# Optimization experiments

Hardware: AMD Instinct MI355X
Metric: run time of the kernel (lower is better)

## Reference

```python
import jax, jax.numpy as jnp
import numpy as np

B, C, H, W = 8, 64, 112, 112
O, K, PAD, STRIDE = 64, 3, 1, 1
KK = K * K
OH = (H - K + 2 * PAD) // STRIDE + 1
OW = (W - K + 2 * PAD) // STRIDE + 1
L = OH * OW  # number of patches


def setup_inputs() -> dict:
    key = jax.random.key(0)
    k1, k2, k3 = jax.random.split(key, 3)
    x = jax.random.normal(k1, (B, C, H, W), dtype=jnp.float32)
    weight = jax.random.normal(k2, (O, C, K, K), dtype=jnp.float32)
    # one uniformly random kernel position to zero out, per patch (nums=1)
    mask_idx = jax.random.randint(k3, (L,), 0, KK, dtype=jnp.int32)
    return {"x": x, "weight": weight, "mask_idx": mask_idx}


def reference(x, weight, mask_idx):
    b = x.shape[0]
    # im2col: [b, C*KK, OH, OW], feature dim ordered channel-major (c, kh, kw)
    # which matches torch.nn.Unfold ordering.
    patches = jax.lax.conv_general_dilated_patches(
        x, (K, K), (STRIDE, STRIDE), ((PAD, PAD), (PAD, PAD)))
    patches = patches.reshape(b, C * KK, L)  # [b, CK, L]

    # Per-patch mask over kernel positions, tiled across channels
    # (equivalent to mask.repeat(1, in_channels) in the original).
    mask = jnp.ones((L, KK), dtype=x.dtype).at[jnp.arange(L), mask_idx].set(0.0)
    mask_full = jnp.tile(mask, (1, C))  # [L, C*KK]

    # weight.view(O, -1).t() -> [CK, O]; masking the weight rows per patch is
    # mathematically identical to masking the unfolded input per patch, which
    # avoids materializing the [L, CK, O] masked weight tensor.
    w2 = weight.reshape(O, C * KK).T  # [CK, O]
    out = jnp.einsum('bkl,lk,ko->bol', patches, mask_full, w2)  # [b, O, L]
    return out.reshape(b, O, OH, OW)
```

## Files before the change

kernel.cpp:

```cpp
#include <hip/hip_runtime.h>
#include <hip/hip_bf16.h>
#include <cstdint>

#define Bn 8
#define Cn 64
#define Hn 112
#define Wn 112
#define On 64
#define Ln (Hn * Wn)
#define HP 114
#define WP 114

typedef __attribute__((ext_vector_type(4))) float f32x4;
typedef __attribute__((ext_vector_type(8))) short bf16x8;
typedef __attribute__((ext_vector_type(4))) unsigned int u32x4;

__device__ __forceinline__ unsigned short f2bf(float f) {
    unsigned u = __float_as_uint(f);
    unsigned r = 0x7fffu + ((u >> 16) & 1u);
    return (unsigned short)((u + r) >> 16);
}

__global__ __launch_bounds__(128) void prepad_nhwc(const float* __restrict__ x,
                                                   unsigned short* __restrict__ xpad) {
    int bh = blockIdx.x;
    int b = bh / HP, hp = bh - b * HP;
    int wp = threadIdx.x;
    if (wp >= WP) return;
    int h = hp - 1, w = wp - 1;
    bool inb = (h >= 0) & (h < Hn) & (w >= 0) & (w < Wn);
    const float* src = x + ((size_t)b * Cn) * (Hn * Wn) + (inb ? (h * Wn + w) : 0);
    unsigned int buf[32];
#pragma unroll
    for (int c = 0; c < Cn; c += 2) {
        float v0 = src[(size_t)c * (Hn * Wn)];
        float v1 = src[(size_t)(c + 1) * (Hn * Wn)];
        if (!inb) { v0 = 0.f; v1 = 0.f; }
        buf[c >> 1] = (unsigned)f2bf(v0) | ((unsigned)f2bf(v1) << 16);
    }
    u32x4* dst = reinterpret_cast<u32x4*>(xpad + ((size_t)(b * HP + hp) * WP + wp) * Cn);
#pragma unroll
    for (int i = 0; i < 8; i++) {
        u32x4 v;
        v[0] = buf[i * 4 + 0]; v[1] = buf[i * 4 + 1];
        v[2] = buf[i * 4 + 2]; v[3] = buf[i * 4 + 3];
        dst[i] = v;
    }
}

__global__ __launch_bounds__(64) void wpack_kernel(const float* __restrict__ w,
                                                   unsigned short* __restrict__ wpk) {
    int idx = blockIdx.x;
    int ki = idx & 1, of = (idx >> 1) & 3, p = idx >> 3;
    int lane = threadIdx.x;
    int o = of * 16 + (lane & 15);
    int cb = ki * 32 + (lane >> 4) * 8;
    unsigned int pk[4];
#pragma unroll
    for (int j = 0; j < 4; j++) {
        float v0 = w[((size_t)o * Cn + cb + 2 * j) * 9 + p];
        float v1 = w[((size_t)o * Cn + cb + 2 * j + 1) * 9 + p];
        pk[j] = (unsigned)f2bf(v0) | ((unsigned)f2bf(v1) << 16);
    }
    u32x4 v; v[0] = pk[0]; v[1] = pk[1]; v[2] = pk[2]; v[3] = pk[3];
    reinterpret_cast<u32x4*>(wpk)[idx * 64 + lane] = v;
}

__global__ __launch_bounds__(512) void conv_main(const unsigned short* __restrict__ xpad,
                                                 const unsigned short* __restrict__ wpk,
                                                 const int* __restrict__ mask_idx,
                                                 float* __restrict__ out) {
    __shared__ char xs[4 * WP * Cn * 2];

    int blk = blockIdx.x;
    int b = blk / 98;
    int lt = blk - b * 98;
    int l0 = lt * 128;
    int oh0 = l0 / Wn;

    int tid = threadIdx.x;

    const u32x4* src = reinterpret_cast<const u32x4*>(
        xpad + ((size_t)(b * HP + oh0) * WP) * Cn);
#pragma unroll
    for (int it = 0; it < 8; it++) {
        int idx = tid + it * 512;
        if (idx < 4 * WP * 8) {
            u32x4 v = src[idx];
            int rw = idx >> 3;
            int wq = rw % WP;
            int off = (idx * 16) ^ ((wq & 7) << 4);
            *reinterpret_cast<u32x4*>(xs + off) = v;
        }
    }

    int wave = tid >> 6, lane = tid & 63;
    int wr = wave >> 2;
    int wc = wave & 3;
    int g = lane >> 4, li = lane & 15;

    int pit0 = wc * 32 + li;
    int pit1 = pit0 + 16;
    int lg0 = l0 + pit0, lg1 = l0 + pit1;
    int oh_0 = lg0 / Wn, ow_0 = lg0 - oh_0 * Wn;
    int oh_1 = lg1 / Wn, ow_1 = lg1 - oh_1 * Wn;
    int r0 = oh_0 - oh0, r1 = oh_1 - oh0;
    int mv0 = mask_idx[lg0], mv1 = mask_idx[lg1];

    f32x4 acc[2][2] = {};
    const u32x4* wv = reinterpret_cast<const u32x4*>(wpk);
    const u32x4 vzero = {0u, 0u, 0u, 0u};

    __syncthreads();

    for (int p = 0; p < 9; p++) {
        int dh = p / 3, dw = p - dh * 3;

        bf16x8 af[2][2];
#pragma unroll
        for (int mi = 0; mi < 2; mi++)
#pragma unroll
            for (int ki = 0; ki < 2; ki++) {
                int fidx = p * 8 + (wr * 2 + mi) * 2 + ki;
                u32x4 raw = wv[fidx * 64 + lane];
                af[mi][ki] = *reinterpret_cast<bf16x8*>(&raw);
            }

        int wq0 = ow_0 + dw, wq1 = ow_1 + dw;
        int ba0 = ((((r0 + dh) * WP + wq0) << 7) + (g << 4)) ^ ((wq0 & 7) << 4);
        int ba1 = ((((r1 + dh) * WP + wq1) << 7) + (g << 4)) ^ ((wq1 & 7) << 4);
        u32x4 v00 = *reinterpret_cast<const u32x4*>(xs + ba0);
        u32x4 v01 = *reinterpret_cast<const u32x4*>(xs + (ba0 ^ 64));
        u32x4 v10 = *reinterpret_cast<const u32x4*>(xs + ba1);
        u32x4 v11 = *reinterpret_cast<const u32x4*>(xs + (ba1 ^ 64));
        if (mv0 == p) { v00 = vzero; v01 = vzero; }
        if (mv1 == p) { v10 = vzero; v11 = vzero; }
        bf16x8 bf00 = *reinterpret_cast<bf16x8*>(&v00);
        bf16x8 bf01 = *reinterpret_cast<bf16x8*>(&v01);
        bf16x8 bf10 = *reinterpret_cast<bf16x8*>(&v10);
        bf16x8 bf11 = *reinterpret_cast<bf16x8*>(&v11);

#pragma unroll
        for (int mi = 0; mi < 2; mi++) {
            acc[mi][0] = __builtin_amdgcn_mfma_f32_16x16x32_bf16(af[mi][0], bf00, acc[mi][0], 0, 0, 0);
            acc[mi][0] = __builtin_amdgcn_mfma_f32_16x16x32_bf16(af[mi][1], bf01, acc[mi][0], 0, 0, 0);
            acc[mi][1] = __builtin_amdgcn_mfma_f32_16x16x32_bf16(af[mi][0], bf10, acc[mi][1], 0, 0, 0);
            acc[mi][1] = __builtin_amdgcn_mfma_f32_16x16x32_bf16(af[mi][1], bf11, acc[mi][1], 0, 0, 0);
        }
    }

#pragma unroll
    for (int mi = 0; mi < 2; mi++) {
#pragma unroll
        for (int ni = 0; ni < 2; ni++) {
            int o = wr * 32 + mi * 16 + g * 4;
            int lpix = l0 + wc * 32 + ni * 16 + li;
            float* dst = out + ((size_t)(b * On + o)) * Ln + lpix;
#pragma unroll
            for (int r = 0; r < 4; r++) dst[(size_t)r * Ln] = acc[mi][ni][r];
        }
    }
}

extern "C" void kernel_launch(void* const* d_in, const int* in_sizes, int n_in,
                              void* d_out, int out_size, void* d_ws, size_t ws_size,
                              hipStream_t stream) {
    const float* x    = (const float*)d_in[0];
    const float* w    = (const float*)d_in[1];
    const int*   mask = (const int*)d_in[2];
    float* out = (float*)d_out;

    unsigned short* xpad = (unsigned short*)d_ws;
    unsigned short* wpk  = (unsigned short*)((char*)d_ws +
                                             (size_t)Bn * HP * WP * Cn * 2);

    prepad_nhwc <<<Bn * HP, 128, 0, stream>>>(x, xpad);
    wpack_kernel<<<72,      64,  0, stream>>>(w, wpk);
    conv_main   <<<Bn * 98, 512, 0, stream>>>(xpad, wpk, mask, out);
}
```

Before: 112.8 us.

## Fuse NCHW-to-padded-NHWC bf16 conversion into conv kernel, prefetch weights

Drops the separate prepad kernel. The conv kernel now reads fp32 NCHW input directly, converts it to bf16 and writes the padded, swizzled tile straight into shared memory. This removes a launch and the write-then-read of the padded intermediate buffer, but each input row is loaded redundantly by neighbouring tiles (four rows per 128-pixel tile), and the global reads are strided across channels. The change also software-prefetches the next kernel position's weight fragments into registers, and reorders block indexing so the batch index varies fastest.

```diff
diff --git a/kernel.cpp b/kernel.cpp
--- a/kernel.cpp
+++ b/kernel.cpp
@@ -15,37 +15,10 @@
 typedef __attribute__((ext_vector_type(8))) short bf16x8;
 typedef __attribute__((ext_vector_type(4))) unsigned int u32x4;
 
-__device__ __forceinline__ unsigned short f2bf(float f) {
+__device__ __forceinline__ unsigned f2bf(float f) {
     unsigned u = __float_as_uint(f);
     unsigned r = 0x7fffu + ((u >> 16) & 1u);
-    return (unsigned short)((u + r) >> 16);
-}
-
-__global__ __launch_bounds__(128) void prepad_nhwc(const float* __restrict__ x,
-                                                   unsigned short* __restrict__ xpad) {
-    int bh = blockIdx.x;
-    int b = bh / HP, hp = bh - b * HP;
-    int wp = threadIdx.x;
-    if (wp >= WP) return;
-    int h = hp - 1, w = wp - 1;
-    bool inb = (h >= 0) & (h < Hn) & (w >= 0) & (w < Wn);
-    const float* src = x + ((size_t)b * Cn) * (Hn * Wn) + (inb ? (h * Wn + w) : 0);
-    unsigned int buf[32];
-#pragma unroll
-    for (int c = 0; c < Cn; c += 2) {
-        float v0 = src[(size_t)c * (Hn * Wn)];
-        float v1 = src[(size_t)(c + 1) * (Hn * Wn)];
-        if (!inb) { v0 = 0.f; v1 = 0.f; }
-        buf[c >> 1] = (unsigned)f2bf(v0) | ((unsigned)f2bf(v1) << 16);
-    }
-    u32x4* dst = reinterpret_cast<u32x4*>(xpad + ((size_t)(b * HP + hp) * WP + wp) * Cn);
-#pragma unroll
-    for (int i = 0; i < 8; i++) {
-        u32x4 v;
-        v[0] = buf[i * 4 + 0]; v[1] = buf[i * 4 + 1];
-        v[2] = buf[i * 4 + 2]; v[3] = buf[i * 4 + 3];
-        dst[i] = v;
-    }
+    return (u + r) >> 16;
 }
 
 __global__ __launch_bounds__(64) void wpack_kernel(const float* __restrict__ w,
@@ -60,36 +33,49 @@
     for (int j = 0; j < 4; j++) {
         float v0 = w[((size_t)o * Cn + cb + 2 * j) * 9 + p];
         float v1 = w[((size_t)o * Cn + cb + 2 * j + 1) * 9 + p];
-        pk[j] = (unsigned)f2bf(v0) | ((unsigned)f2bf(v1) << 16);
+        pk[j] = f2bf(v0) | (f2bf(v1) << 16);
     }
     u32x4 v; v[0] = pk[0]; v[1] = pk[1]; v[2] = pk[2]; v[3] = pk[3];
     reinterpret_cast<u32x4*>(wpk)[idx * 64 + lane] = v;
 }
 
-__global__ __launch_bounds__(512) void conv_main(const unsigned short* __restrict__ xpad,
-                                                 const unsigned short* __restrict__ wpk,
-                                                 const int* __restrict__ mask_idx,
-                                                 float* __restrict__ out) {
+__global__ __launch_bounds__(512) void conv_fused(const float* __restrict__ x,
+                                                  const unsigned short* __restrict__ wpk,
+                                                  const int* __restrict__ mask_idx,
+                                                  float* __restrict__ out) {
     __shared__ char xs[4 * WP * Cn * 2];
 
-    int blk = blockIdx.x;
-    int b = blk / 98;
-    int lt = blk - b * 98;
+    int b  = blockIdx.x & 7;
+    int lt = blockIdx.x >> 3;
     int l0 = lt * 128;
     int oh0 = l0 / Wn;
 
     int tid = threadIdx.x;
 
-    const u32x4* src = reinterpret_cast<const u32x4*>(
-        xpad + ((size_t)(b * HP + oh0) * WP) * Cn);
+    const float* xb = x + (size_t)b * Cn * Hn * Wn;
 #pragma unroll
-    for (int it = 0; it < 8; it++) {
-        int idx = tid + it * 512;
-        if (idx < 4 * WP * 8) {
-            u32x4 v = src[idx];
-            int rw = idx >> 3;
-            int wq = rw % WP;
-            int off = (idx * 16) ^ ((wq & 7) << 4);
+    for (int it = 0; it < 8; ++it) {
+        int q = tid + it * 512;
+        if (q < 4 * 8 * WP) {
+            int row = q / (8 * WP);
+            int rem = q - row * (8 * WP);
+            int c8  = rem / WP;
+            int wp  = rem - c8 * WP;
+            int h = oh0 + row - 1;
+            int w = wp - 1;
+            bool inb = ((unsigned)h < (unsigned)Hn) & ((unsigned)w < (unsigned)Wn);
+            const float* s = xb + ((size_t)(c8 * 8) * Hn + (inb ? h : 0)) * Wn + (inb ? w : 0);
+            unsigned pk[4];
+#pragma unroll
+            for (int j = 0; j < 4; ++j) {
+                float v0 = s[(size_t)(2 * j)     * (Hn * Wn)];
+                float v1 = s[(size_t)(2 * j + 1) * (Hn * Wn)];
+                if (!inb) { v0 = 0.f; v1 = 0.f; }
+                pk[j] = f2bf(v0) | (f2bf(v1) << 16);
+            }
+            int qs = (row * WP + wp) * 8 + c8;
+            int off = (qs * 16) ^ ((wp & 7) << 4);
+            u32x4 v; v[0] = pk[0]; v[1] = pk[1]; v[2] = pk[2]; v[3] = pk[3];
             *reinterpret_cast<u32x4*>(xs + off) = v;
         }
     }
@@ -111,20 +97,26 @@
     const u32x4* wv = reinterpret_cast<const u32x4*>(wpk);
     const u32x4 vzero = {0u, 0u, 0u, 0u};
 
+    u32x4 an[4];
+#pragma unroll
+    for (int f = 0; f < 4; ++f) an[f] = wv[(wr * 4 + f) * 64 + lane];
+
     __syncthreads();
 
-    for (int p = 0; p < 9; p++) {
+    for (int p = 0; p < 9; ++p) {
         int dh = p / 3, dw = p - dh * 3;
 
+        u32x4 ac[4] = {an[0], an[1], an[2], an[3]};
+        if (p < 8) {
+#pragma unroll
+            for (int f = 0; f < 4; ++f)
+                an[f] = wv[((p + 1) * 8 + wr * 4 + f) * 64 + lane];
+        }
         bf16x8 af[2][2];
-#pragma unroll
-        for (int mi = 0; mi < 2; mi++)
-#pragma unroll
-            for (int ki = 0; ki < 2; ki++) {
-                int fidx = p * 8 + (wr * 2 + mi) * 2 + ki;
-                u32x4 raw = wv[fidx * 64 + lane];
-                af[mi][ki] = *reinterpret_cast<bf16x8*>(&raw);
-            }
+        af[0][0] = *reinterpret_cast<bf16x8*>(&ac[0]);
+        af[0][1] = *reinterpret_cast<bf16x8*>(&ac[1]);
+        af[1][0] = *reinterpret_cast<bf16x8*>(&ac[2]);
+        af[1][1] = *reinterpret_cast<bf16x8*>(&ac[3]);
 
         int wq0 = ow_0 + dw, wq1 = ow_1 + dw;
         int ba0 = ((((r0 + dh) * WP + wq0) << 7) + (g << 4)) ^ ((wq0 & 7) << 4);
@@ -170,11 +162,8 @@
     const int*   mask = (const int*)d_in[2];
     float* out = (float*)d_out;
 
-    unsigned short* xpad = (unsigned short*)d_ws;
-    unsigned short* wpk  = (unsigned short*)((char*)d_ws +
-                                             (size_t)Bn * HP * WP * Cn * 2);
+    unsigned short* wpk = (unsigned short*)d_ws;
 
-    prepad_nhwc <<<Bn * HP, 128, 0, stream>>>(x, xpad);
     wpack_kernel<<<72,      64,  0, stream>>>(w, wpk);
-    conv_main   <<<Bn * 98, 512, 0, stream>>>(xpad, wpk, mask, out);
+    conv_fused  <<<Bn * 98, 512, 0, stream>>>(x, wpk, mask, out);
 }
```

After: 97.48 us. 1.16x faster.
